# Kernel optimization log

Measured on AMD Instinct MI355X. Metric: run time of the kernel, lower is better.

Reference implementation:

```python
import jax, jax.numpy as jnp
import numpy as np

N, E, B = 100000, 1200000, 512
IN_DIM, HID, K, NCLS = 64, 64, 3, 10


def setup_inputs() -> dict:
    key = jax.random.key(0)
    ks = jax.random.split(key, 10)
    features = jax.random.normal(ks[0], (N, IN_DIM), jnp.float32)
    edge_src = jax.random.randint(ks[1], (E,), 0, N)
    edge_dst = jax.random.randint(ks[2], (E,), 0, N)
    graph_ids = jnp.sort(jax.random.randint(ks[3], (N,), 0, B))
    s1 = float(1.0 / np.sqrt(IN_DIM))
    W1 = jax.random.uniform(ks[4], (IN_DIM, HID), jnp.float32, -s1, s1)
    b1 = jnp.zeros((HID,), jnp.float32)
    s2 = float(1.0 / np.sqrt(HID))
    W2 = jax.random.uniform(ks[5], (HID, HID), jnp.float32, -s2, s2)
    b2 = jnp.zeros((HID,), jnp.float32)
    s3 = float(1.0 / np.sqrt(HID * 3))
    cw = jax.random.uniform(ks[6], (HID, HID, 3), jnp.float32, -s3, s3)
    cb = jax.random.uniform(ks[7], (HID,), jnp.float32, -s3, s3)
    Wc = jax.random.uniform(ks[8], (HID, NCLS), jnp.float32, -s2, s2)
    bc = jax.random.uniform(ks[9], (NCLS,), jnp.float32, -s2, s2)
    return dict(features=features, edge_src=edge_src, edge_dst=edge_dst,
                graph_ids=graph_ids, num_graphs=B,
                W1=W1, b1=b1, W2=W2, b2=b2, cw=cw, cb=cb, Wc=Wc, bc=bc)


def graph_conv(h, src, dst, W, b, n_nodes):
    # DGL GraphConv, norm='both', allow_zero_in_degree (degrees clamped to 1)
    ones = jnp.ones((src.shape[0],), h.dtype)
    out_deg = jnp.zeros((n_nodes,), h.dtype).at[src].add(ones)
    in_deg = jnp.zeros((n_nodes,), h.dtype).at[dst].add(ones)
    norm_s = jax.lax.rsqrt(jnp.clip(out_deg, 1.0, None))
    norm_d = jax.lax.rsqrt(jnp.clip(in_deg, 1.0, None))
    m = (h * norm_s[:, None]) @ W  # weight first; math identical to agg-first
    agg = jnp.zeros((n_nodes, W.shape[1]), h.dtype).at[dst].add(m[src])
    return agg * norm_d[:, None] + b


def sort_pool(h, gid, num_graphs, k):
    # DGL SortPooling: sort each node's features ascending along feature dim,
    # then take top-k nodes per graph by last feature value (descending),
    # zero-padding graphs with < k nodes. Output [num_graphs, k*D].
    hs = jnp.sort(h, axis=-1)
    key = hs[:, -1]
    order = jnp.lexsort((-key, gid))  # gid asc, key desc
    gid_s = gid[order]
    hs_s = hs[order]
    n = gid.shape[0]
    start = jnp.full((num_graphs,), n).at[gid_s].min(jnp.arange(n))
    rank = jnp.arange(n) - start[gid_s]  # within-graph rank by key desc
    mask = rank < k
    slot = gid_s * k + jnp.clip(rank, 0, k - 1)
    out = jnp.zeros((num_graphs * k, hs.shape[-1]), h.dtype).at[slot].add(
        jnp.where(mask[:, None], hs_s, jnp.zeros((), h.dtype)))
    return out.reshape(num_graphs, k * hs.shape[-1])


def reference(features, edge_src, edge_dst, graph_ids, num_graphs,
              W1, b1, W2, b2, cw, cb, Wc, bc):
    n = features.shape[0]
    h = jax.nn.relu(graph_conv(features, edge_src, edge_dst, W1, b1, n))
    h = jax.nn.relu(graph_conv(h, edge_src, edge_dst, W2, b2, n))
    p = sort_pool(h, graph_ids, num_graphs, K)          # [B, K*HID]
    x = p.reshape(num_graphs, HID, K)                    # faithful torch reshape
    # Conv1d(kernel=3, stride=1) on length-3 input -> length-1 output
    y = jax.nn.relu(jnp.einsum('bct,oct->bo', x, cw) + cb)
    return y @ Wc + bc
```

## Files before the change

kernel.cpp:

```cpp
#include <hip/hip_runtime.h>
#include <hip/hip_bf16.h>


#define PART_H 50176
#define QPART_H (PART_H / 4)
#define PART_F 25088
#define QUART_F (PART_F / 4)
#define MCH  64

__global__ void __launch_bounds__(256) k_histgemm(
    const int* __restrict__ esrc, const int* __restrict__ edst,
    unsigned char* __restrict__ hd, unsigned char* __restrict__ hs,
    const float* __restrict__ in, const float* __restrict__ W,
    float* __restrict__ mout, int N, int E, int PH, int histBlocks) {
  __shared__ float smem[12800];
  const int t = threadIdx.x;
  if (blockIdx.x < histBlocks) {
    unsigned int* lc = (unsigned int*)smem;
    const int b = blockIdx.x;
    const int half = PH * MCH;
    const int a = b / half;
    const int r = b % half;
    const int p = r % PH;
    const int m = r / PH;
    const int* __restrict__ arr = a ? esrc : edst;
    unsigned char* __restrict__ outp = a ? hs : hd;
    const int base = p * PART_H;
    const int lim = min(PART_H, N - base);
    for (int i = t; i < QPART_H; i += 256) lc[i] = 0u;
    __syncthreads();
    const long long cb = (long long)m * E / MCH;
    const long long ce = (long long)(m + 1) * E / MCH;
    const long long a0 = min((cb + 3) & ~3LL, ce);
    const long long nv = (ce - a0) >> 2;
    for (long long e = cb + t; e < a0; e += 256) {
      int d = arr[e] - base;
      if ((unsigned)d < (unsigned)lim) atomicAdd(&lc[d >> 2], 1u << ((d & 3) * 8));
    }
    const int4* __restrict__ a4p = (const int4*)(arr + a0);
    for (long long i = t; i < nv; i += 256) {
      int4 v4 = a4p[i];
      int d;
      d = v4.x - base; if ((unsigned)d < (unsigned)lim) atomicAdd(&lc[d >> 2], 1u << ((d & 3) * 8));
      d = v4.y - base; if ((unsigned)d < (unsigned)lim) atomicAdd(&lc[d >> 2], 1u << ((d & 3) * 8));
      d = v4.z - base; if ((unsigned)d < (unsigned)lim) atomicAdd(&lc[d >> 2], 1u << ((d & 3) * 8));
      d = v4.w - base; if ((unsigned)d < (unsigned)lim) atomicAdd(&lc[d >> 2], 1u << ((d & 3) * 8));
    }
    for (long long e = a0 + (nv << 2) + t; e < ce; e += 256) {
      int d = arr[e] - base;
      if ((unsigned)d < (unsigned)lim) atomicAdd(&lc[d >> 2], 1u << ((d & 3) * 8));
    }
    __syncthreads();
    unsigned char* slice = outp + ((size_t)p * MCH + m) * PART_H;
    for (int i = t; i < lim; i += 256)
      slice[i] = (unsigned char)((lc[i >> 2] >> ((i & 3) * 8)) & 0xffu);
  } else {
    float* Wl = smem;
    float* Ac = smem + 4096;
    const int ch = (t & 7) * 8;
    const int nb = (t >> 3) * 4;
    for (int i = t; i < 1024; i += 256)
      ((float4*)Wl)[i] = ((const float4*)W)[i];
    const int gb = blockIdx.x - histBlocks;
    const int ng = gridDim.x - histBlocks;
    const int NT = (N + 127) >> 7;
    for (int tile = gb; tile < NT; tile += ng) {
      const int vbase = tile << 7;
      __syncthreads();
      for (int i = t; i < 2048; i += 256) {
        const int r = i >> 4;
        const int c = (i & 15) * 4;
        const int v = vbase + r;
        float4 val = make_float4(0.f, 0.f, 0.f, 0.f);
        if (v < N) val = *(const float4*)(in + (size_t)v * 64 + c);
        Ac[(c + 0) * 136 + r] = val.x;
        Ac[(c + 1) * 136 + r] = val.y;
        Ac[(c + 2) * 136 + r] = val.z;
        Ac[(c + 3) * 136 + r] = val.w;
      }
      __syncthreads();
      float acc[4][8];
#pragma unroll
      for (int j = 0; j < 4; ++j)
#pragma unroll
        for (int c = 0; c < 8; ++c) acc[j][c] = 0.f;
      for (int k = 0; k < 64; k += 4) {
#pragma unroll
        for (int kk = 0; kk < 4; ++kk) {
          const float4 aa = *(const float4*)&Ac[(k + kk) * 136 + nb];
          const float4 w0 = *(const float4*)&Wl[(k + kk) * 64 + ch];
          const float4 w1 = *(const float4*)&Wl[(k + kk) * 64 + ch + 4];
          const float an[4] = {aa.x, aa.y, aa.z, aa.w};
          const float wn[8] = {w0.x, w0.y, w0.z, w0.w, w1.x, w1.y, w1.z, w1.w};
#pragma unroll
          for (int j = 0; j < 4; ++j)
#pragma unroll
            for (int c = 0; c < 8; ++c)
              acc[j][c] = fmaf(an[j], wn[c], acc[j][c]);
        }
      }
#pragma unroll
      for (int j = 0; j < 4; ++j) {
        const int v = vbase + nb + j;
        if (v < N) {
          float4 o0, o1;
          o0.x = acc[j][0]; o0.y = acc[j][1]; o0.z = acc[j][2]; o0.w = acc[j][3];
          o1.x = acc[j][4]; o1.y = acc[j][5]; o1.z = acc[j][6]; o1.w = acc[j][7];
          *(float4*)(mout + (size_t)v * 64 + ch)     = o0;
          *(float4*)(mout + (size_t)v * 64 + ch + 4) = o1;
        }
      }
    }
  }
}

__global__ void __launch_bounds__(256) k_offscan(
    unsigned char* __restrict__ hd, const unsigned char* __restrict__ hs,
    int* __restrict__ deg_d, float* __restrict__ norm_s, float* __restrict__ norm_d,
    int* __restrict__ gstart, int* __restrict__ rowptr, int* __restrict__ bsum,
    int B, int N) {
  __shared__ unsigned long long part[32][8];
  __shared__ unsigned long long spart[32][8];
  __shared__ int sums[256];
  const int t = threadIdx.x;
  const int s = t >> 3;
  const int c = t & 7;
  const int nb0 = blockIdx.x * 256;
  const int v0 = nb0 + s * 8;
  const int vt = nb0 + t;
  if (vt < B) gstart[vt] = 0x7f7f7f7f;
  const size_t rb = (size_t)(v0 / PART_H) * MCH * PART_H + (size_t)(v0 % PART_H);
  unsigned long long* __restrict__ hd8 = (unsigned long long*)(hd + rb);
  const unsigned long long* __restrict__ hs8 = (const unsigned long long*)(hs + rb);
  const size_t st8 = PART_H / 8;
  const int m0 = c * 8;
  const bool act = (v0 < N);
  unsigned long long vals[8];
  unsigned long long tsum = 0ull, hsum = 0ull;
  if (act) {
#pragma unroll
    for (int k = 0; k < 8; ++k) {
      vals[k] = hd8[(size_t)(m0 + k) * st8];
      tsum += vals[k];
      hsum += hs8[(size_t)(m0 + k) * st8];
    }
  }
  part[s][c] = tsum;
  spart[s][c] = hsum;
  __syncthreads();
  if (act) {
    unsigned long long run = 0ull;
#pragma unroll
    for (int cc = 0; cc < 8; ++cc)
      if (cc < c) run += part[s][cc];
#pragma unroll
    for (int k = 0; k < 8; ++k) {
      const unsigned long long w = vals[k];
      hd8[(size_t)(m0 + k) * st8] = run;
      run += w;
    }
  }
  unsigned long long dt = 0ull, ht = 0ull;
#pragma unroll
  for (int cc = 0; cc < 8; ++cc) {
    dt += part[t >> 3][cc];
    ht += spart[t >> 3][cc];
  }
  int dg = 0;
  if (vt < N) {
    dg = (int)((dt >> (8 * (t & 7))) & 0xffull);
    const int so = (int)((ht >> (8 * (t & 7))) & 0xffull);
    deg_d[vt] = dg;
    norm_d[vt] = rsqrtf((float)max(dg, 1));
    norm_s[vt] = rsqrtf((float)max(so, 1));
  }
  sums[t] = dg;
  __syncthreads();
  for (int off = 1; off < 256; off <<= 1) {
    int x = (t >= off) ? sums[t - off] : 0;
    __syncthreads();
    sums[t] += x;
    __syncthreads();
  }
  if (vt < N) rowptr[vt] = sums[t] - dg;
  if (t == 255) bsum[blockIdx.x] = sums[255];
}

__global__ void k_scan2(int* __restrict__ bsum, int nb) {
  __shared__ int sh[512];
  const int t = threadIdx.x;
  const int v = (t < nb) ? bsum[t] : 0;
  sh[t] = v;
  __syncthreads();
  for (int off = 1; off < 512; off <<= 1) {
    int x = (t >= off) ? sh[t - off] : 0;
    __syncthreads();
    sh[t] += x;
    __syncthreads();
  }
  if (t < nb) bsum[t] = sh[t] - v;
}

__global__ void k_fill2(const int* __restrict__ esrc, const int* __restrict__ edst,
                        const unsigned char* __restrict__ hd, const int* __restrict__ rowptr,
                        const int* __restrict__ bsum, int* __restrict__ csr,
                        int N, int E, int PF) {
  __shared__ unsigned int cur4[QUART_F];
  const int b = blockIdx.x;
  const int p = b % PF;
  const int m = b / PF;
  const int base = p * PART_F;
  const int lim = min(PART_F, N - base);
  const unsigned char* slice = hd + ((size_t)(p >> 1) * MCH + m) * PART_H
                                  + (size_t)(p & 1) * PART_F;
  const unsigned int* slice4 = (const unsigned int*)slice;
  for (int i = threadIdx.x; i < QUART_F; i += blockDim.x) cur4[i] = slice4[i];
  __syncthreads();
  const int* __restrict__ rp = rowptr + base;
  const long long cb = (long long)m * E / MCH;
  const long long ce = (long long)(m + 1) * E / MCH;
  const long long a0 = min((cb + 3) & ~3LL, ce);
  const long long nv = (ce - a0) >> 2;
  for (long long e = cb + threadIdx.x; e < a0; e += blockDim.x) {
    int d = edst[e] - base;
    if ((unsigned)d < (unsigned)lim) {
      unsigned int old = atomicAdd(&cur4[d >> 2], 1u << ((d & 3) * 8));
      csr[rp[d] + bsum[(base + d) >> 8] + ((old >> ((d & 3) * 8)) & 0xff)] = esrc[e];
    }
  }
  const int4* __restrict__ d4p = (const int4*)(edst + a0);
  const int4* __restrict__ s4p = (const int4*)(esrc + a0);
  for (long long i = threadIdx.x; i < nv; i += blockDim.x) {
    int4 d4 = d4p[i];
    int4 s4 = s4p[i];
    int d;
    d = d4.x - base;
    if ((unsigned)d < (unsigned)lim) {
      unsigned int old = atomicAdd(&cur4[d >> 2], 1u << ((d & 3) * 8));
      csr[rp[d] + bsum[(base + d) >> 8] + ((old >> ((d & 3) * 8)) & 0xff)] = s4.x;
    }
    d = d4.y - base;
    if ((unsigned)d < (unsigned)lim) {
      unsigned int old = atomicAdd(&cur4[d >> 2], 1u << ((d & 3) * 8));
      csr[rp[d] + bsum[(base + d) >> 8] + ((old >> ((d & 3) * 8)) & 0xff)] = s4.y;
    }
    d = d4.z - base;
    if ((unsigned)d < (unsigned)lim) {
      unsigned int old = atomicAdd(&cur4[d >> 2], 1u << ((d & 3) * 8));
      csr[rp[d] + bsum[(base + d) >> 8] + ((old >> ((d & 3) * 8)) & 0xff)] = s4.z;
    }
    d = d4.w - base;
    if ((unsigned)d < (unsigned)lim) {
      unsigned int old = atomicAdd(&cur4[d >> 2], 1u << ((d & 3) * 8));
      csr[rp[d] + bsum[(base + d) >> 8] + ((old >> ((d & 3) * 8)) & 0xff)] = s4.w;
    }
  }
  for (long long e = a0 + (nv << 2) + threadIdx.x; e < ce; e += blockDim.x) {
    int d = edst[e] - base;
    if ((unsigned)d < (unsigned)lim) {
      unsigned int old = atomicAdd(&cur4[d >> 2], 1u << ((d & 3) * 8));
      csr[rp[d] + bsum[(base + d) >> 8] + ((old >> ((d & 3) * 8)) & 0xff)] = esrc[e];
    }
  }
}

__global__ void __launch_bounds__(256) k_gemm64(
    const float* __restrict__ in, const float* __restrict__ norm,
    const float* __restrict__ W, float* __restrict__ out, int N) {
  __shared__ float Wl[4096];
  __shared__ float Ac[64 * 136];
  const int t = threadIdx.x;
  const int ch = (t & 7) * 8;
  const int nb = (t >> 3) * 4;
  for (int i = t; i < 1024; i += 256)
    ((float4*)Wl)[i] = ((const float4*)W)[i];
  const int NT = (N + 127) >> 7;
  for (int tile = blockIdx.x; tile < NT; tile += gridDim.x) {
    const int vbase = tile << 7;
    __syncthreads();
    for (int i = t; i < 2048; i += 256) {
      const int r = i >> 4;
      const int c = (i & 15) * 4;
      const int v = vbase + r;
      float4 val = make_float4(0.f, 0.f, 0.f, 0.f);
      if (v < N) val = *(const float4*)(in + (size_t)v * 64 + c);
      Ac[(c + 0) * 136 + r] = val.x;
      Ac[(c + 1) * 136 + r] = val.y;
      Ac[(c + 2) * 136 + r] = val.z;
      Ac[(c + 3) * 136 + r] = val.w;
    }
    __syncthreads();
    float acc[4][8];
#pragma unroll
    for (int j = 0; j < 4; ++j)
#pragma unroll
      for (int c = 0; c < 8; ++c) acc[j][c] = 0.f;
    for (int k = 0; k < 64; k += 4) {
#pragma unroll
      for (int kk = 0; kk < 4; ++kk) {
        const float4 aa = *(const float4*)&Ac[(k + kk) * 136 + nb];
        const float4 w0 = *(const float4*)&Wl[(k + kk) * 64 + ch];
        const float4 w1 = *(const float4*)&Wl[(k + kk) * 64 + ch + 4];
        const float an[4] = {aa.x, aa.y, aa.z, aa.w};
        const float wn[8] = {w0.x, w0.y, w0.z, w0.w, w1.x, w1.y, w1.z, w1.w};
#pragma unroll
        for (int j = 0; j < 4; ++j)
#pragma unroll
          for (int c = 0; c < 8; ++c)
            acc[j][c] = fmaf(an[j], wn[c], acc[j][c]);
      }
    }
#pragma unroll
    for (int j = 0; j < 4; ++j) {
      const int v = vbase + nb + j;
      if (v < N) {
        const float nm = norm[v];
        float4 o0, o1;
        o0.x = acc[j][0] * nm; o0.y = acc[j][1] * nm;
        o0.z = acc[j][2] * nm; o0.w = acc[j][3] * nm;
        o1.x = acc[j][4] * nm; o1.y = acc[j][5] * nm;
        o1.z = acc[j][6] * nm; o1.w = acc[j][7] * nm;
        *(float4*)(out + (size_t)v * 64 + ch)     = o0;
        *(float4*)(out + (size_t)v * 64 + ch + 4) = o1;
      }
    }
  }
}

__global__ void k_gather(const float* __restrict__ m, const int* __restrict__ rowptr,
                         const int* __restrict__ bsum,
                         const int* __restrict__ deg, const float* __restrict__ norm_d,
                         const float* __restrict__ bias, const int* __restrict__ csr,
                         const float* __restrict__ nsrc,
                         const int* __restrict__ gid, int* __restrict__ gstart,
                         float* __restrict__ h, float* __restrict__ key, int N) {
  const int wpb = blockDim.x >> 6;
  const int nwaves = gridDim.x * wpb;
  const int lane = threadIdx.x & 63;
  const int chb = (lane & 7) * 8;
  const int grp = lane >> 3;
  const float4 b0 = *(const float4*)(bias + chb);
  const float4 b1 = *(const float4*)(bias + chb + 4);
  for (int w = blockIdx.x * wpb + (threadIdx.x >> 6); w < N; w += nwaves) {
    if (gid != nullptr && lane == 0) {
      int g = gid[w];
      if (w == 0 || gid[w - 1] != g) gstart[g] = w;
    }
    const int start = rowptr[w] + bsum[w >> 8];
    const int cnt = deg[w];
    float4 a00 = make_float4(0.f, 0.f, 0.f, 0.f);
    float4 a01 = make_float4(0.f, 0.f, 0.f, 0.f);
    float4 a10 = make_float4(0.f, 0.f, 0.f, 0.f);
    float4 a11 = make_float4(0.f, 0.f, 0.f, 0.f);
    int i = grp;
    if (nsrc != nullptr) {
      for (; i + 8 < cnt; i += 16) {
        int s0 = csr[start + i];
        int s1 = csr[start + i + 8];
        float n0 = nsrc[s0], n1 = nsrc[s1];
        const float* r0 = m + (size_t)s0 * 64 + chb;
        const float* r1 = m + (size_t)s1 * 64 + chb;
        const float4 v00 = *(const float4*)r0;
        const float4 v01 = *(const float4*)(r0 + 4);
        const float4 v10 = *(const float4*)r1;
        const float4 v11 = *(const float4*)(r1 + 4);
        a00.x = fmaf(v00.x, n0, a00.x); a00.y = fmaf(v00.y, n0, a00.y);
        a00.z = fmaf(v00.z, n0, a00.z); a00.w = fmaf(v00.w, n0, a00.w);
        a01.x = fmaf(v01.x, n0, a01.x); a01.y = fmaf(v01.y, n0, a01.y);
        a01.z = fmaf(v01.z, n0, a01.z); a01.w = fmaf(v01.w, n0, a01.w);
        a10.x = fmaf(v10.x, n1, a10.x); a10.y = fmaf(v10.y, n1, a10.y);
        a10.z = fmaf(v10.z, n1, a10.z); a10.w = fmaf(v10.w, n1, a10.w);
        a11.x = fmaf(v11.x, n1, a11.x); a11.y = fmaf(v11.y, n1, a11.y);
        a11.z = fmaf(v11.z, n1, a11.z); a11.w = fmaf(v11.w, n1, a11.w);
      }
      if (i < cnt) {
        int s0 = csr[start + i];
        float n0 = nsrc[s0];
        const float* r0 = m + (size_t)s0 * 64 + chb;
        const float4 v00 = *(const float4*)r0;
        const float4 v01 = *(const float4*)(r0 + 4);
        a00.x = fmaf(v00.x, n0, a00.x); a00.y = fmaf(v00.y, n0, a00.y);
        a00.z = fmaf(v00.z, n0, a00.z); a00.w = fmaf(v00.w, n0, a00.w);
        a01.x = fmaf(v01.x, n0, a01.x); a01.y = fmaf(v01.y, n0, a01.y);
        a01.z = fmaf(v01.z, n0, a01.z); a01.w = fmaf(v01.w, n0, a01.w);
      }
    } else {
      for (; i + 8 < cnt; i += 16) {
        int s0 = csr[start + i];
        int s1 = csr[start + i + 8];
        const float* r0 = m + (size_t)s0 * 64 + chb;
        const float* r1 = m + (size_t)s1 * 64 + chb;
        const float4 v00 = *(const float4*)r0;
        const float4 v01 = *(const float4*)(r0 + 4);
        const float4 v10 = *(const float4*)r1;
        const float4 v11 = *(const float4*)(r1 + 4);
        a00.x += v00.x; a00.y += v00.y; a00.z += v00.z; a00.w += v00.w;
        a01.x += v01.x; a01.y += v01.y; a01.z += v01.z; a01.w += v01.w;
        a10.x += v10.x; a10.y += v10.y; a10.z += v10.z; a10.w += v10.w;
        a11.x += v11.x; a11.y += v11.y; a11.z += v11.z; a11.w += v11.w;
      }
      if (i < cnt) {
        int s0 = csr[start + i];
        const float* r0 = m + (size_t)s0 * 64 + chb;
        const float4 v00 = *(const float4*)r0;
        const float4 v01 = *(const float4*)(r0 + 4);
        a00.x += v00.x; a00.y += v00.y; a00.z += v00.z; a00.w += v00.w;
        a01.x += v01.x; a01.y += v01.y; a01.z += v01.z; a01.w += v01.w;
      }
    }
    a00.x += a10.x; a00.y += a10.y; a00.z += a10.z; a00.w += a10.w;
    a01.x += a11.x; a01.y += a11.y; a01.z += a11.z; a01.w += a11.w;
#pragma unroll
    for (int off = 8; off <= 32; off <<= 1) {
      a00.x += __shfl_xor(a00.x, off, 64);
      a00.y += __shfl_xor(a00.y, off, 64);
      a00.z += __shfl_xor(a00.z, off, 64);
      a00.w += __shfl_xor(a00.w, off, 64);
      a01.x += __shfl_xor(a01.x, off, 64);
      a01.y += __shfl_xor(a01.y, off, 64);
      a01.z += __shfl_xor(a01.z, off, 64);
      a01.w += __shfl_xor(a01.w, off, 64);
    }
    const float nd = norm_d[w];
    float4 o0, o1;
    o0.x = fmaxf(fmaf(a00.x, nd, b0.x), 0.f);
    o0.y = fmaxf(fmaf(a00.y, nd, b0.y), 0.f);
    o0.z = fmaxf(fmaf(a00.z, nd, b0.z), 0.f);
    o0.w = fmaxf(fmaf(a00.w, nd, b0.w), 0.f);
    o1.x = fmaxf(fmaf(a01.x, nd, b1.x), 0.f);
    o1.y = fmaxf(fmaf(a01.y, nd, b1.y), 0.f);
    o1.z = fmaxf(fmaf(a01.z, nd, b1.z), 0.f);
    o1.w = fmaxf(fmaf(a01.w, nd, b1.w), 0.f);
    if (grp == 0) {
      *(float4*)(h + (size_t)w * 64 + chb)     = o0;
      *(float4*)(h + (size_t)w * 64 + chb + 4) = o1;
    }
    if (key != nullptr) {
      float mx = fmaxf(fmaxf(fmaxf(o0.x, o0.y), fmaxf(o0.z, o0.w)),
                       fmaxf(fmaxf(o1.x, o1.y), fmaxf(o1.z, o1.w)));
#pragma unroll
      for (int off = 1; off < 8; off <<= 1) mx = fmaxf(mx, __shfl_xor(mx, off, 64));
      if (lane == 0) key[w] = mx;
    }
  }
}

__global__ void __launch_bounds__(256) k_tail(
    const float* __restrict__ key, const int* __restrict__ gstart,
    const float* __restrict__ h,
    const float* __restrict__ cw, const float* __restrict__ cb,
    const float* __restrict__ Wc, const float* __restrict__ bc,
    float* __restrict__ out, int B, int N) {
  __shared__ int sel[3];
  __shared__ float prow[192];
  const int b = blockIdx.x;
  const int wid = threadIdx.x >> 6;
  const int lane = threadIdx.x & 63;

  if (wid == 0) {
    const int gs = gstart[b];
    int g2 = b + 1;
    while (g2 < B && gstart[g2] >= N) ++g2;
    const int ns = (g2 < B) ? gstart[g2] : N;
    const int s = gs;
    const int c = (gs < N) ? (ns - gs) : 0;
    float v0 = -1.f, v1 = -1.f, v2 = -1.f;
    int i0 = 0x7fffffff, i1 = 0x7fffffff, i2 = 0x7fffffff;
    for (int i = s + lane; i < s + c; i += 64) {
      float kv = key[i];
      if (kv > v0 || (kv == v0 && i < i0)) {
        v2 = v1; i2 = i1; v1 = v0; i1 = i0; v0 = kv; i0 = i;
      } else if (kv > v1 || (kv == v1 && i < i1)) {
        v2 = v1; i2 = i1; v1 = kv; i1 = i;
      } else if (kv > v2 || (kv == v2 && i < i2)) {
        v2 = kv; i2 = i;
      }
    }
    int ptr = 0;
    for (int r = 0; r < 3; ++r) {
      float mv = (ptr == 0) ? v0 : (ptr == 1) ? v1 : (ptr == 2) ? v2 : -1.f;
      int   mi = (ptr == 0) ? i0 : (ptr == 1) ? i1 : (ptr == 2) ? i2 : 0x7fffffff;
      float bv = mv; int bi = mi;
#pragma unroll
      for (int off = 32; off; off >>= 1) {
        float ov = __shfl_xor(bv, off, 64);
        int   oi = __shfl_xor(bi, off, 64);
        if (ov > bv || (ov == bv && oi < bi)) { bv = ov; bi = oi; }
      }
      if (bi == mi && ptr < 3) ptr++;
      if (lane == 0) sel[r] = (bi == 0x7fffffff) ? -1 : bi;
    }
  }
  __syncthreads();
  if (wid < 3) {
    int node = sel[wid];
    float v = 0.f;
    if (node >= 0) {
      v = h[(size_t)node * 64 + lane];
      for (int k2 = 2; k2 <= 64; k2 <<= 1) {
        for (int j = k2 >> 1; j > 0; j >>= 1) {
          float o = __shfl_xor(v, j, 64);
          bool up = ((lane & k2) == 0);
          bool lower = ((lane & j) == 0);
          v = (lower == up) ? fminf(v, o) : fmaxf(v, o);
        }
      }
    }
    prow[wid * 64 + lane] = v;
  }
  __syncthreads();
  if (wid == 0) {
    float y = cb[lane];
    for (int j = 0; j < 192; ++j) y = fmaf(prow[j], cw[lane * 192 + j], y);
    float ry = fmaxf(y, 0.f);
    for (int c = 0; c < 10; ++c) {
      float s = ry * Wc[lane * 10 + c];
#pragma unroll
      for (int off = 32; off; off >>= 1) s += __shfl_xor(s, off, 64);
      if (lane == 0) out[b * 10 + c] = s + bc[c];
    }
  }
}

extern "C" void kernel_launch(void* const* d_in, const int* in_sizes, int n_in,
                              void* d_out, int out_size, void* d_ws, size_t ws_size,
                              hipStream_t stream) {
  const float* features = (const float*)d_in[0];
  const int*   esrc     = (const int*)d_in[1];
  const int*   edst     = (const int*)d_in[2];
  const int*   gid      = (const int*)d_in[3];
  const float* W1 = (const float*)d_in[5];
  const float* b1 = (const float*)d_in[6];
  const float* W2 = (const float*)d_in[7];
  const float* b2 = (const float*)d_in[8];
  const float* cw = (const float*)d_in[9];
  const float* cb = (const float*)d_in[10];
  const float* Wc = (const float*)d_in[11];
  const float* bc = (const float*)d_in[12];
  float* out = (float*)d_out;

  const int N = in_sizes[0] / 64;
  const int E = in_sizes[1];
  const int B = out_size / 10;
  const size_t N64 = (size_t)N * 64;
  const int nscan = (N + 255) / 256;
  const int PH = (N + PART_H - 1) / PART_H;
  const int PF = (N + PART_F - 1) / PART_F;
  const size_t HSZ = (size_t)PH * MCH * PART_H;
  const int NT = (N + 127) / 128;
  const int histBlocks = 2 * PH * MCH;

  float* bufA   = (float*)d_ws;
  float* bufB   = bufA + N64;
  int*   deg_d  = (int*)(bufB + N64);
  float* norm_s = (float*)(deg_d + N);
  float* norm_d = norm_s + N;
  float* key    = norm_d + N;
  int*   rowptr = (int*)(key + N);
  int*   csr    = rowptr + N;
  int*   bsum   = csr + E;
  int*   gstart = bsum + 512;
  unsigned char* hd = (unsigned char*)(((size_t)(gstart + B) + 15) & ~(size_t)15);
  unsigned char* hs = hd + HSZ;

  const int TB = 256;

  k_histgemm<<<histBlocks + NT, TB, 0, stream>>>(esrc, edst, hd, hs,
                                                 features, W1, bufA,
                                                 N, E, PH, histBlocks);
  k_offscan<<<nscan, 256, 0, stream>>>(hd, hs, deg_d, norm_s, norm_d,
                                       gstart, rowptr, bsum, B, N);
  k_scan2<<<1, 512, 0, stream>>>(bsum, nscan);
  k_fill2<<<PF * MCH, TB, 0, stream>>>(esrc, edst, hd, rowptr, bsum, csr, N, E, PF);

  const int GB = 2048;

  k_gather<<<GB, TB, 0, stream>>>(bufA, rowptr, bsum, deg_d, norm_d, b1,
                                  csr, norm_s, nullptr, nullptr,
                                  bufB, nullptr, N);

  k_gemm64<<<NT, TB, 0, stream>>>(bufB, norm_s, W2, bufA, N);
  k_gather<<<GB, TB, 0, stream>>>(bufA, rowptr, bsum, deg_d, norm_d, b2,
                                  csr, nullptr, gid, gstart,
                                  bufB, key, N);

  k_tail<<<B, TB, 0, stream>>>(key, gstart, bufB, cw, cb, Wc, bc, out, B, N);
}
```

Before: 294.2 us.

## Fuse layer-2 weight GEMM into first gather epilogue, widen histogram chunks

Drops the separate k_gemm64 launch. The first gather kernel now multiplies each aggregated, activated row by W2 (kept in shared memory), reduces across lane groups with shuffles, scales by norm_s and writes the result for the second gather. This avoids writing the intermediate hidden layer to memory and reading it back. The histogram chunk count MCH doubles from 64 to 128, the offset scan reads 16 slices per thread instead of 8, and histogram slices are written as 32-bit words instead of bytes. The trade-offs are more histogram blocks and scan work, plus extra shuffle and shared-memory traffic inside the gather.

```diff
diff --git a/kernel.cpp b/kernel.cpp
--- a/kernel.cpp
+++ b/kernel.cpp
@@ -6,7 +6,7 @@
 #define QPART_H (PART_H / 4)
 #define PART_F 25088
 #define QUART_F (PART_F / 4)
-#define MCH  64
+#define MCH  128
 
 __global__ void __launch_bounds__(256) k_histgemm(
     const int* __restrict__ esrc, const int* __restrict__ edst,
@@ -52,7 +52,10 @@
     }
     __syncthreads();
     unsigned char* slice = outp + ((size_t)p * MCH + m) * PART_H;
-    for (int i = t; i < lim; i += 256)
+    unsigned int* slice4 = (unsigned int*)slice;
+    const int lim4 = lim >> 2;
+    for (int i = t; i < lim4; i += 256) slice4[i] = lc[i];
+    for (int i = (lim4 << 2) + t; i < lim; i += 256)
       slice[i] = (unsigned char)((lc[i >> 2] >> ((i & 3) * 8)) & 0xffu);
   } else {
     float* Wl = smem;
@@ -133,13 +136,13 @@
   unsigned long long* __restrict__ hd8 = (unsigned long long*)(hd + rb);
   const unsigned long long* __restrict__ hs8 = (const unsigned long long*)(hs + rb);
   const size_t st8 = PART_H / 8;
-  const int m0 = c * 8;
+  const int m0 = c * 16;
   const bool act = (v0 < N);
-  unsigned long long vals[8];
+  unsigned long long vals[16];
   unsigned long long tsum = 0ull, hsum = 0ull;
   if (act) {
 #pragma unroll
-    for (int k = 0; k < 8; ++k) {
+    for (int k = 0; k < 16; ++k) {
       vals[k] = hd8[(size_t)(m0 + k) * st8];
       tsum += vals[k];
       hsum += hs8[(size_t)(m0 + k) * st8];
@@ -154,7 +157,7 @@
     for (int cc = 0; cc < 8; ++cc)
       if (cc < c) run += part[s][cc];
 #pragma unroll
-    for (int k = 0; k < 8; ++k) {
+    for (int k = 0; k < 16; ++k) {
       const unsigned long long w = vals[k];
       hd8[(size_t)(m0 + k) * st8] = run;
       run += w;
@@ -264,76 +267,16 @@
   }
 }
 
-__global__ void __launch_bounds__(256) k_gemm64(
-    const float* __restrict__ in, const float* __restrict__ norm,
-    const float* __restrict__ W, float* __restrict__ out, int N) {
-  __shared__ float Wl[4096];
-  __shared__ float Ac[64 * 136];
-  const int t = threadIdx.x;
-  const int ch = (t & 7) * 8;
-  const int nb = (t >> 3) * 4;
-  for (int i = t; i < 1024; i += 256)
-    ((float4*)Wl)[i] = ((const float4*)W)[i];
-  const int NT = (N + 127) >> 7;
-  for (int tile = blockIdx.x; tile < NT; tile += gridDim.x) {
-    const int vbase = tile << 7;
-    __syncthreads();
-    for (int i = t; i < 2048; i += 256) {
-      const int r = i >> 4;
-      const int c = (i & 15) * 4;
-      const int v = vbase + r;
-      float4 val = make_float4(0.f, 0.f, 0.f, 0.f);
-      if (v < N) val = *(const float4*)(in + (size_t)v * 64 + c);
-      Ac[(c + 0) * 136 + r] = val.x;
-      Ac[(c + 1) * 136 + r] = val.y;
-      Ac[(c + 2) * 136 + r] = val.z;
-      Ac[(c + 3) * 136 + r] = val.w;
-    }
-    __syncthreads();
-    float acc[4][8];
-#pragma unroll
-    for (int j = 0; j < 4; ++j)
-#pragma unroll
-      for (int c = 0; c < 8; ++c) acc[j][c] = 0.f;
-    for (int k = 0; k < 64; k += 4) {
-#pragma unroll
-      for (int kk = 0; kk < 4; ++kk) {
-        const float4 aa = *(const float4*)&Ac[(k + kk) * 136 + nb];
-        const float4 w0 = *(const float4*)&Wl[(k + kk) * 64 + ch];
-        const float4 w1 = *(const float4*)&Wl[(k + kk) * 64 + ch + 4];
-        const float an[4] = {aa.x, aa.y, aa.z, aa.w};
-        const float wn[8] = {w0.x, w0.y, w0.z, w0.w, w1.x, w1.y, w1.z, w1.w};
-#pragma unroll
-        for (int j = 0; j < 4; ++j)
-#pragma unroll
-          for (int c = 0; c < 8; ++c)
-            acc[j][c] = fmaf(an[j], wn[c], acc[j][c]);
-      }
-    }
-#pragma unroll
-    for (int j = 0; j < 4; ++j) {
-      const int v = vbase + nb + j;
-      if (v < N) {
-        const float nm = norm[v];
-        float4 o0, o1;
-        o0.x = acc[j][0] * nm; o0.y = acc[j][1] * nm;
-        o0.z = acc[j][2] * nm; o0.w = acc[j][3] * nm;
-        o1.x = acc[j][4] * nm; o1.y = acc[j][5] * nm;
-        o1.z = acc[j][6] * nm; o1.w = acc[j][7] * nm;
-        *(float4*)(out + (size_t)v * 64 + ch)     = o0;
-        *(float4*)(out + (size_t)v * 64 + ch + 4) = o1;
-      }
-    }
-  }
-}
-
 __global__ void k_gather(const float* __restrict__ m, const int* __restrict__ rowptr,
                          const int* __restrict__ bsum,
                          const int* __restrict__ deg, const float* __restrict__ norm_d,
                          const float* __restrict__ bias, const int* __restrict__ csr,
                          const float* __restrict__ nsrc,
                          const int* __restrict__ gid, int* __restrict__ gstart,
-                         float* __restrict__ h, float* __restrict__ key, int N) {
+                         float* __restrict__ h, float* __restrict__ key,
+                         const float* __restrict__ W2f, const float* __restrict__ ns2,
+                         int N) {
+  __shared__ float Wl2[4096];
   const int wpb = blockDim.x >> 6;
   const int nwaves = gridDim.x * wpb;
   const int lane = threadIdx.x & 63;
@@ -341,6 +284,11 @@
   const int grp = lane >> 3;
   const float4 b0 = *(const float4*)(bias + chb);
   const float4 b1 = *(const float4*)(bias + chb + 4);
+  if (W2f != nullptr) {
+    for (int i = threadIdx.x; i < 1024; i += 256)
+      ((float4*)Wl2)[i] = ((const float4*)W2f)[i];
+    __syncthreads();
+  }
   for (int w = blockIdx.x * wpb + (threadIdx.x >> 6); w < N; w += nwaves) {
     if (gid != nullptr && lane == 0) {
       int g = gid[w];
@@ -431,16 +379,52 @@
     o1.y = fmaxf(fmaf(a01.y, nd, b1.y), 0.f);
     o1.z = fmaxf(fmaf(a01.z, nd, b1.z), 0.f);
     o1.w = fmaxf(fmaf(a01.w, nd, b1.w), 0.f);
-    if (grp == 0) {
-      *(float4*)(h + (size_t)w * 64 + chb)     = o0;
-      *(float4*)(h + (size_t)w * 64 + chb + 4) = o1;
-    }
-    if (key != nullptr) {
-      float mx = fmaxf(fmaxf(fmaxf(o0.x, o0.y), fmaxf(o0.z, o0.w)),
-                       fmaxf(fmaxf(o1.x, o1.y), fmaxf(o1.z, o1.w)));
-#pragma unroll
-      for (int off = 1; off < 8; off <<= 1) mx = fmaxf(mx, __shfl_xor(mx, off, 64));
-      if (lane == 0) key[w] = mx;
+    if (W2f != nullptr) {
+      const float hr[8] = {o0.x, o0.y, o0.z, o0.w, o1.x, o1.y, o1.z, o1.w};
+      float4 pA = make_float4(0.f, 0.f, 0.f, 0.f);
+      float4 pB = make_float4(0.f, 0.f, 0.f, 0.f);
+      const int ob = grp << 3;
+#pragma unroll
+      for (int j = 0; j < 8; ++j) {
+        const float hv = hr[j];
+        const float4 wA = *(const float4*)&Wl2[(chb + j) * 64 + ob];
+        const float4 wB = *(const float4*)&Wl2[(chb + j) * 64 + ob + 4];
+        pA.x = fmaf(hv, wA.x, pA.x); pA.y = fmaf(hv, wA.y, pA.y);
+        pA.z = fmaf(hv, wA.z, pA.z); pA.w = fmaf(hv, wA.w, pA.w);
+        pB.x = fmaf(hv, wB.x, pB.x); pB.y = fmaf(hv, wB.y, pB.y);
+        pB.z = fmaf(hv, wB.z, pB.z); pB.w = fmaf(hv, wB.w, pB.w);
+      }
+#pragma unroll
+      for (int off = 1; off <= 4; off <<= 1) {
+        pA.x += __shfl_xor(pA.x, off, 64);
+        pA.y += __shfl_xor(pA.y, off, 64);
+        pA.z += __shfl_xor(pA.z, off, 64);
+        pA.w += __shfl_xor(pA.w, off, 64);
+        pB.x += __shfl_xor(pB.x, off, 64);
+        pB.y += __shfl_xor(pB.y, off, 64);
+        pB.z += __shfl_xor(pB.z, off, 64);
+        pB.w += __shfl_xor(pB.w, off, 64);
+      }
+      if ((lane & 7) == 0) {
+        const float ns = ns2[w];
+        float4 sA, sB;
+        sA.x = pA.x * ns; sA.y = pA.y * ns; sA.z = pA.z * ns; sA.w = pA.w * ns;
+        sB.x = pB.x * ns; sB.y = pB.y * ns; sB.z = pB.z * ns; sB.w = pB.w * ns;
+        *(float4*)(h + (size_t)w * 64 + ob)     = sA;
+        *(float4*)(h + (size_t)w * 64 + ob + 4) = sB;
+      }
+    } else {
+      if (grp == 0) {
+        *(float4*)(h + (size_t)w * 64 + chb)     = o0;
+        *(float4*)(h + (size_t)w * 64 + chb + 4) = o1;
+      }
+      if (key != nullptr) {
+        float mx = fmaxf(fmaxf(fmaxf(o0.x, o0.y), fmaxf(o0.z, o0.w)),
+                         fmaxf(fmaxf(o1.x, o1.y), fmaxf(o1.z, o1.w)));
+#pragma unroll
+        for (int off = 1; off < 8; off <<= 1) mx = fmaxf(mx, __shfl_xor(mx, off, 64));
+        if (lane == 0) key[w] = mx;
+      }
     }
   }
 }
@@ -577,12 +561,11 @@
 
   k_gather<<<GB, TB, 0, stream>>>(bufA, rowptr, bsum, deg_d, norm_d, b1,
                                   csr, norm_s, nullptr, nullptr,
-                                  bufB, nullptr, N);
-
-  k_gemm64<<<NT, TB, 0, stream>>>(bufB, norm_s, W2, bufA, N);
-  k_gather<<<GB, TB, 0, stream>>>(bufA, rowptr, bsum, deg_d, norm_d, b2,
+                                  bufB, nullptr, W2, norm_s, N);
+
+  k_gather<<<GB, TB, 0, stream>>>(bufB, rowptr, bsum, deg_d, norm_d, b2,
                                   csr, nullptr, gid, gstart,
-                                  bufB, key, N);
-
-  k_tail<<<B, TB, 0, stream>>>(key, gstart, bufB, cw, cb, Wc, bc, out, B, N);
-}
+                                  bufA, key, nullptr, nullptr, N);
+
+  k_tail<<<B, TB, 0, stream>>>(key, gstart, bufA, cw, cb, Wc, bc, out, B, N);
+}
```

New measurement: 345.9 us. 17.6% more time.

## Rebalance degree histogram chunking and add nontemporal accesses in gather

Applied to the files above, without the earlier changes.

The in-degree histogram now splits the edge list into 128 chunks per partition, while the out-degree histogram uses only 32. Only the in-degree counts need per-chunk offsets for the CSR fill; the out-degree counts only feed the normalisation. The offset scan is reworked to match, reading 16 in-degree slices and 4 out-degree slices per thread. Histogram slices are now written out as 32-bit words instead of single bytes. The gather kernel uses nontemporal loads for rowptr/deg/csr/norm_d and nontemporal stores for h and key, to keep streaming data out of the cache. The extra in-degree chunks raise histogram block count and scan work, traded against more parallelism and a lower risk of byte-counter overflow per chunk.

```diff
diff --git a/kernel.cpp b/kernel.cpp
--- a/kernel.cpp
+++ b/kernel.cpp
@@ -6,7 +6,10 @@
 #define QPART_H (PART_H / 4)
 #define PART_F 25088
 #define QUART_F (PART_F / 4)
-#define MCH  64
+#define MCH  128
+#define MCHS 32
+
+typedef float f4nt __attribute__((ext_vector_type(4)));
 
 __global__ void __launch_bounds__(256) k_histgemm(
     const int* __restrict__ esrc, const int* __restrict__ edst,
@@ -18,9 +21,10 @@
   if (blockIdx.x < histBlocks) {
     unsigned int* lc = (unsigned int*)smem;
     const int b = blockIdx.x;
-    const int half = PH * MCH;
-    const int a = b / half;
-    const int r = b % half;
+    const int dblk = PH * MCH;
+    const int a = (b < dblk) ? 0 : 1;
+    const int r = a ? (b - dblk) : b;
+    const int mch = a ? MCHS : MCH;
     const int p = r % PH;
     const int m = r / PH;
     const int* __restrict__ arr = a ? esrc : edst;
@@ -29,8 +33,8 @@
     const int lim = min(PART_H, N - base);
     for (int i = t; i < QPART_H; i += 256) lc[i] = 0u;
     __syncthreads();
-    const long long cb = (long long)m * E / MCH;
-    const long long ce = (long long)(m + 1) * E / MCH;
+    const long long cb = (long long)m * E / mch;
+    const long long ce = (long long)(m + 1) * E / mch;
     const long long a0 = min((cb + 3) & ~3LL, ce);
     const long long nv = (ce - a0) >> 2;
     for (long long e = cb + t; e < a0; e += 256) {
@@ -51,8 +55,11 @@
       if ((unsigned)d < (unsigned)lim) atomicAdd(&lc[d >> 2], 1u << ((d & 3) * 8));
     }
     __syncthreads();
-    unsigned char* slice = outp + ((size_t)p * MCH + m) * PART_H;
-    for (int i = t; i < lim; i += 256)
+    unsigned char* slice = outp + ((size_t)p * mch + m) * PART_H;
+    unsigned int* slice4 = (unsigned int*)slice;
+    const int lim4 = lim >> 2;
+    for (int i = t; i < lim4; i += 256) slice4[i] = lc[i];
+    for (int i = (lim4 << 2) + t; i < lim; i += 256)
       slice[i] = (unsigned char)((lc[i >> 2] >> ((i & 3) * 8)) & 0xffu);
   } else {
     float* Wl = smem;
@@ -129,21 +136,24 @@
   const int v0 = nb0 + s * 8;
   const int vt = nb0 + t;
   if (vt < B) gstart[vt] = 0x7f7f7f7f;
-  const size_t rb = (size_t)(v0 / PART_H) * MCH * PART_H + (size_t)(v0 % PART_H);
+  const size_t rb  = (size_t)(v0 / PART_H) * MCH  * PART_H + (size_t)(v0 % PART_H);
+  const size_t rbs = (size_t)(v0 / PART_H) * MCHS * PART_H + (size_t)(v0 % PART_H);
   unsigned long long* __restrict__ hd8 = (unsigned long long*)(hd + rb);
-  const unsigned long long* __restrict__ hs8 = (const unsigned long long*)(hs + rb);
+  const unsigned long long* __restrict__ hs8 = (const unsigned long long*)(hs + rbs);
   const size_t st8 = PART_H / 8;
-  const int m0 = c * 8;
+  const int m0 = c * 16;
+  const int m0s = c * 4;
   const bool act = (v0 < N);
-  unsigned long long vals[8];
+  unsigned long long vals[16];
   unsigned long long tsum = 0ull, hsum = 0ull;
   if (act) {
 #pragma unroll
-    for (int k = 0; k < 8; ++k) {
+    for (int k = 0; k < 16; ++k) {
       vals[k] = hd8[(size_t)(m0 + k) * st8];
       tsum += vals[k];
-      hsum += hs8[(size_t)(m0 + k) * st8];
-    }
+    }
+#pragma unroll
+    for (int k = 0; k < 4; ++k) hsum += hs8[(size_t)(m0s + k) * st8];
   }
   part[s][c] = tsum;
   spart[s][c] = hsum;
@@ -154,7 +164,7 @@
     for (int cc = 0; cc < 8; ++cc)
       if (cc < c) run += part[s][cc];
 #pragma unroll
-    for (int k = 0; k < 8; ++k) {
+    for (int k = 0; k < 16; ++k) {
       const unsigned long long w = vals[k];
       hd8[(size_t)(m0 + k) * st8] = run;
       run += w;
@@ -346,8 +356,8 @@
       int g = gid[w];
       if (w == 0 || gid[w - 1] != g) gstart[g] = w;
     }
-    const int start = rowptr[w] + bsum[w >> 8];
-    const int cnt = deg[w];
+    const int start = __builtin_nontemporal_load(rowptr + w) + bsum[w >> 8];
+    const int cnt = __builtin_nontemporal_load(deg + w);
     float4 a00 = make_float4(0.f, 0.f, 0.f, 0.f);
     float4 a01 = make_float4(0.f, 0.f, 0.f, 0.f);
     float4 a10 = make_float4(0.f, 0.f, 0.f, 0.f);
@@ -355,8 +365,8 @@
     int i = grp;
     if (nsrc != nullptr) {
       for (; i + 8 < cnt; i += 16) {
-        int s0 = csr[start + i];
-        int s1 = csr[start + i + 8];
+        int s0 = __builtin_nontemporal_load(csr + start + i);
+        int s1 = __builtin_nontemporal_load(csr + start + i + 8);
         float n0 = nsrc[s0], n1 = nsrc[s1];
         const float* r0 = m + (size_t)s0 * 64 + chb;
         const float* r1 = m + (size_t)s1 * 64 + chb;
@@ -371,10 +381,10 @@
         a10.x = fmaf(v10.x, n1, a10.x); a10.y = fmaf(v10.y, n1, a10.y);
         a10.z = fmaf(v10.z, n1, a10.z); a10.w = fmaf(v10.w, n1, a10.w);
         a11.x = fmaf(v11.x, n1, a11.x); a11.y = fmaf(v11.y, n1, a11.y);
-        a11.z = fmaf(v11.z, n1, a11.z); a11.w = fmaf(v11.w, n1, a11.w);
+        a11.w = fmaf(v11.w, n1, a11.w); a11.z = fmaf(v11.z, n1, a11.z);
       }
       if (i < cnt) {
-        int s0 = csr[start + i];
+        int s0 = __builtin_nontemporal_load(csr + start + i);
         float n0 = nsrc[s0];
         const float* r0 = m + (size_t)s0 * 64 + chb;
         const float4 v00 = *(const float4*)r0;
@@ -386,8 +396,8 @@
       }
     } else {
       for (; i + 8 < cnt; i += 16) {
-        int s0 = csr[start + i];
-        int s1 = csr[start + i + 8];
+        int s0 = __builtin_nontemporal_load(csr + start + i);
+        int s1 = __builtin_nontemporal_load(csr + start + i + 8);
         const float* r0 = m + (size_t)s0 * 64 + chb;
         const float* r1 = m + (size_t)s1 * 64 + chb;
         const float4 v00 = *(const float4*)r0;
@@ -400,7 +410,7 @@
         a11.x += v11.x; a11.y += v11.y; a11.z += v11.z; a11.w += v11.w;
       }
       if (i < cnt) {
-        int s0 = csr[start + i];
+        int s0 = __builtin_nontemporal_load(csr + start + i);
         const float* r0 = m + (size_t)s0 * 64 + chb;
         const float4 v00 = *(const float4*)r0;
         const float4 v01 = *(const float4*)(r0 + 4);
@@ -421,7 +431,7 @@
       a01.z += __shfl_xor(a01.z, off, 64);
       a01.w += __shfl_xor(a01.w, off, 64);
     }
-    const float nd = norm_d[w];
+    const float nd = __builtin_nontemporal_load(norm_d + w);
     float4 o0, o1;
     o0.x = fmaxf(fmaf(a00.x, nd, b0.x), 0.f);
     o0.y = fmaxf(fmaf(a00.y, nd, b0.y), 0.f);
@@ -432,15 +442,15 @@
     o1.z = fmaxf(fmaf(a01.z, nd, b1.z), 0.f);
     o1.w = fmaxf(fmaf(a01.w, nd, b1.w), 0.f);
     if (grp == 0) {
-      *(float4*)(h + (size_t)w * 64 + chb)     = o0;
-      *(float4*)(h + (size_t)w * 64 + chb + 4) = o1;
+      __builtin_nontemporal_store(*(const f4nt*)&o0, (f4nt*)(h + (size_t)w * 64 + chb));
+      __builtin_nontemporal_store(*(const f4nt*)&o1, (f4nt*)(h + (size_t)w * 64 + chb + 4));
     }
     if (key != nullptr) {
       float mx = fmaxf(fmaxf(fmaxf(o0.x, o0.y), fmaxf(o0.z, o0.w)),
                        fmaxf(fmaxf(o1.x, o1.y), fmaxf(o1.z, o1.w)));
 #pragma unroll
       for (int off = 1; off < 8; off <<= 1) mx = fmaxf(mx, __shfl_xor(mx, off, 64));
-      if (lane == 0) key[w] = mx;
+      if (lane == 0) __builtin_nontemporal_store(mx, key + w);
     }
   }
 }
@@ -546,9 +556,10 @@
   const int nscan = (N + 255) / 256;
   const int PH = (N + PART_H - 1) / PART_H;
   const int PF = (N + PART_F - 1) / PART_F;
-  const size_t HSZ = (size_t)PH * MCH * PART_H;
+  const size_t HSZD = (size_t)PH * MCH  * PART_H;
+  const size_t HSZS = (size_t)PH * MCHS * PART_H;
   const int NT = (N + 127) / 128;
-  const int histBlocks = 2 * PH * MCH;
+  const int histBlocks = PH * (MCH + MCHS);
 
   float* bufA   = (float*)d_ws;
   float* bufB   = bufA + N64;
@@ -561,7 +572,7 @@
   int*   bsum   = csr + E;
   int*   gstart = bsum + 512;
   unsigned char* hd = (unsigned char*)(((size_t)(gstart + B) + 15) & ~(size_t)15);
-  unsigned char* hs = hd + HSZ;
+  unsigned char* hs = hd + HSZD;
 
   const int TB = 256;
 
```

Result: slower. 380.5 us (+29.3%).
